# Optimization experiments

Hardware: AMD Instinct MI355X
Metric: run time of the kernel (lower is better)

Reference implementation:

```python
import jax, jax.numpy as jnp
import numpy as np

VOCAB = 32000
D = 256
B, S = 16, 128


def setup_inputs() -> dict:
    key = jax.random.key(0)
    ks = jax.random.split(key, 8)
    s = 1.0 / np.sqrt(D)
    return {
        "X": jax.random.randint(ks[0], (B, S), 0, VOCAB),
        "emb": jax.random.normal(ks[1], (VOCAB, D), dtype=jnp.float32),
        "Wl": jax.random.uniform(ks[2], (D, D), jnp.float32, -s, s),
        "bl": jax.random.uniform(ks[3], (D,), jnp.float32, -s, s),
        "Wr": jax.random.uniform(ks[4], (D, D), jnp.float32, -s, s),
        "br": jax.random.uniform(ks[5], (D,), jnp.float32, -s, s),
        "Wrel": jax.random.uniform(ks[6], (D, D), jnp.float32, -s, s),
        "brel": jax.random.uniform(ks[7], (D,), jnp.float32, -s, s),
    }


def reference(X, emb, Wl, bl, Wr, br, Wrel, brel):
    # X: [B,S] int -> embed [B,S,D]
    e = emb[X]
    L = jnp.einsum("bsd,de->bse", e, Wl.T) + bl  # left projection per token
    R = jnp.einsum("bsd,de->bse", e, Wr.T) + br  # right projection per token
    # all-pairs relu(L_i + R_j): [B,S,S,D]
    pair = jax.nn.relu(L[:, :, None, :] + R[:, None, :, :])
    # relation is affine, so mean over S^2 pairs commutes with it (same math,
    # one [B,D] GEMM instead of B*S^2 tiny ones)
    pooled = pair.mean(axis=(1, 2))  # [B,D]
    return pooled @ Wrel.T + brel
```

## Files before the change

kernel.cpp:

```cpp
#include <hip/hip_runtime.h>
#include <hip/hip_bf16.h>

#define DD 256
#define SS 128
#define BB 16

typedef __attribute__((ext_vector_type(8))) short bf16x8;
typedef __attribute__((ext_vector_type(4))) short bf16x4;
typedef __attribute__((ext_vector_type(4))) float f32x4;

static __device__ __forceinline__ short f2bf(float f) {
    __hip_bfloat16 h = __float2bfloat16(f);
    return *reinterpret_cast<short*>(&h);
}

static __device__ __forceinline__ int swz(int r, int kb) {
    return r * 512 + (kb ^ ((r & 7) << 4));
}


__global__ __launch_bounds__(512, 2) void k_fused(
    const int* __restrict__ X, const float* __restrict__ emb,
    const float* __restrict__ Wl, const float* __restrict__ bl,
    const float* __restrict__ Wr, const float* __restrict__ br,
    float* __restrict__ sumLg, float* __restrict__ sumRg,
    float* __restrict__ absS)
{
    __shared__ __align__(16) short Ebf[128 * 256];
    __shared__ __align__(16) float Lcol[16 * 132];
    __shared__ __align__(16) float Rcol[16 * 132];
    __shared__ float redA[512];
    __shared__ float redwL[8 * 16];
    __shared__ float redwR[8 * 16];

    const int tid  = threadIdx.x;
    const int bx   = (blockIdx.x & 7) * 32 + (blockIdx.x >> 3);
    const int b    = bx >> 4;
    const int dc   = bx & 15;
    const int dr0  = dc * 16;
    const int w    = __builtin_amdgcn_readfirstlane(tid >> 6);
    const int lane = tid & 63;
    const int lr   = lane & 15, lk = lane >> 4;

    int tok[16];
#pragma unroll
    for (int i = 0; i < 8; ++i) tok[i]     = X[b * SS + i * 8 + w];
#pragma unroll
    for (int i = 0; i < 8; ++i) tok[8 + i] = X[b * SS + 64 + i * 8 + w];

    float4 ga[16];
#pragma unroll
    for (int i = 0; i < 16; ++i)
        ga[i] = *(const float4*)&emb[(size_t)tok[i] * DD + lane * 4];

    bf16x8 wlf[8], wrf[8];
    {
        const float* plw = Wl + (size_t)(dr0 + lr) * DD + lk * 8;
        const float* prw = Wr + (size_t)(dr0 + lr) * DD + lk * 8;
#pragma unroll
        for (int ks = 0; ks < 8; ++ks) {
            float4 f0 = *(const float4*)(plw + ks * 32);
            float4 f1 = *(const float4*)(plw + ks * 32 + 4);
            bf16x8 p;
            p[0]=f2bf(f0.x); p[1]=f2bf(f0.y); p[2]=f2bf(f0.z); p[3]=f2bf(f0.w);
            p[4]=f2bf(f1.x); p[5]=f2bf(f1.y); p[6]=f2bf(f1.z); p[7]=f2bf(f1.w);
            wlf[ks] = p;
            f0 = *(const float4*)(prw + ks * 32);
            f1 = *(const float4*)(prw + ks * 32 + 4);
            p[0]=f2bf(f0.x); p[1]=f2bf(f0.y); p[2]=f2bf(f0.z); p[3]=f2bf(f0.w);
            p[4]=f2bf(f1.x); p[5]=f2bf(f1.y); p[6]=f2bf(f1.z); p[7]=f2bf(f1.w);
            wrf[ks] = p;
        }
    }

    char* Eb = (char*)Ebf;
#pragma unroll
    for (int i = 0; i < 8; ++i) {
        bf16x4 p; p[0]=f2bf(ga[i].x); p[1]=f2bf(ga[i].y); p[2]=f2bf(ga[i].z); p[3]=f2bf(ga[i].w);
        *(bf16x4*)(Eb + swz(i * 8 + w, lane * 8)) = p;
    }
#pragma unroll
    for (int i = 0; i < 8; ++i) {
        bf16x4 p; p[0]=f2bf(ga[8+i].x); p[1]=f2bf(ga[8+i].y); p[2]=f2bf(ga[8+i].z); p[3]=f2bf(ga[8+i].w);
        *(bf16x4*)(Eb + swz(64 + i * 8 + w, lane * 8)) = p;
    }
    __syncthreads();

    f32x4 accL = {0.f,0.f,0.f,0.f}, accR = accL;
#pragma unroll
    for (int ks = 0; ks < 8; ++ks) {
        bf16x8 a = *(bf16x8*)(Eb + swz(w * 16 + lr, ks * 64 + lk * 16));
        accL = __builtin_amdgcn_mfma_f32_16x16x32_bf16(a, wlf[ks], accL, 0, 0, 0);
        accR = __builtin_amdgcn_mfma_f32_16x16x32_bf16(a, wrf[ks], accR, 0, 0, 0);
    }
    const float blv = bl[dr0 + lr];
    const float brv = br[dr0 + lr];
#pragma unroll
    for (int reg = 0; reg < 4; ++reg) {
        int s = w * 16 + lk * 4 + reg;
        Lcol[lr * 132 + s] = accL[reg] + blv;
        Rcol[lr * 132 + s] = accR[reg] + brv;
    }
    float tl = (accL[0] + accL[1]) + (accL[2] + accL[3]) + blv * 4.0f;
    float tr = (accR[0] + accR[1]) + (accR[2] + accR[3]) + brv * 4.0f;
    tl += __shfl_xor(tl, 16);  tr += __shfl_xor(tr, 16);
    tl += __shfl_xor(tl, 32);  tr += __shfl_xor(tr, 32);
    if (lane < 16) { redwL[w * 16 + lr] = tl; redwR[w * 16 + lr] = tr; }
    __syncthreads();

    const int d = tid & 15, jg = tid >> 4;
    float rr[4];
    *(float4*)rr = *(float4*)&Rcol[d * 132 + jg * 4];

    float a0 = 0.f, a1 = 0.f, a2 = 0.f, a3 = 0.f;
    for (int i = 0; i < 128; i += 4) {
        float4 l4 = *(float4*)&Lcol[d * 132 + i];
#pragma unroll
        for (int q = 0; q < 4; ++q) {
            a0 += fabsf(l4.x + rr[q]);
            a1 += fabsf(l4.y + rr[q]);
            a2 += fabsf(l4.z + rr[q]);
            a3 += fabsf(l4.w + rr[q]);
        }
    }
    redA[tid] = (a0 + a1) + (a2 + a3);
    __syncthreads();

    if (tid < 16) {
        float sa = 0.f;
#pragma unroll
        for (int g = 0; g < 32; ++g) sa += redA[g * 16 + tid];
        float sl = 0.f, sr = 0.f;
#pragma unroll
        for (int wv = 0; wv < 8; ++wv) {
            sl += redwL[wv * 16 + tid];
            sr += redwR[wv * 16 + tid];
        }
        absS [b * DD + dr0 + tid] = sa;
        sumLg[b * DD + dr0 + tid] = sl;
        sumRg[b * DD + dr0 + tid] = sr;
    }
}

__global__ __launch_bounds__(256) void k_final(
    const float* __restrict__ sumLg, const float* __restrict__ sumRg,
    const float* __restrict__ absS,
    const float* __restrict__ Wrel, const float* __restrict__ brel,
    float* __restrict__ out)
{
    __shared__ float plds[DD];
    const int tid = threadIdx.x;
    const int b   = blockIdx.x;

    float sl = sumLg[b * DD + tid];
    float sr = sumRg[b * DD + tid];
    float sa = absS [b * DD + tid];

    plds[tid] = (128.0f * (sl + sr) + sa) * (1.0f / 32768.0f);
    __syncthreads();

    float acc = brel[tid];
    const float4* w4 = (const float4*)(Wrel + (size_t)tid * DD);
#pragma unroll
    for (int k4 = 0; k4 < DD / 4; ++k4) {
        float4 p = *(float4*)&plds[k4 * 4];
        float4 w = w4[k4];
        acc = fmaf(p.x, w.x, acc);
        acc = fmaf(p.y, w.y, acc);
        acc = fmaf(p.z, w.z, acc);
        acc = fmaf(p.w, w.w, acc);
    }
    out[b * DD + tid] = acc;
}

extern "C" void kernel_launch(void* const* d_in, const int* in_sizes, int n_in,
                              void* d_out, int out_size, void* d_ws, size_t ws_size,
                              hipStream_t stream) {
    const int*   X    = (const int*)d_in[0];
    const float* emb  = (const float*)d_in[1];
    const float* Wl   = (const float*)d_in[2];
    const float* bl   = (const float*)d_in[3];
    const float* Wr   = (const float*)d_in[4];
    const float* br   = (const float*)d_in[5];
    const float* Wrel = (const float*)d_in[6];
    const float* brel = (const float*)d_in[7];
    float* out = (float*)d_out;

    float* ws    = (float*)d_ws;
    float* sumLg = ws;
    float* sumRg = sumLg + BB * DD;
    float* absS  = sumRg + BB * DD;

    k_fused<<<BB * 16, 512, 0, stream>>>(X, emb, Wl, bl, Wr, br,
                                         sumLg, sumRg, absS);
    k_final<<<BB, 256, 0, stream>>>(sumLg, sumRg, absS, Wrel, brel, out);
}
```

Measured before the change: 27.89 us.

## Gather embeddings straight into LDS via global_load_lds; split-K the final GEMV

The embedding gather now uses global_load_lds to copy fp32 rows directly into LDS. The XOR swizzle is applied on the global source address, and each wave waits on vmcnt for only its own rows, replacing the register staging, bf16 conversion and block barrier. The bf16 conversion moves to the MFMA operand load, and LDS storage doubles to fp32, which limits the fused kernel to one block per CU. The final Wrel GEMV uses 1024 threads with a 4-way K split and preloaded weights to shorten the per-thread dependent FMA chain.

Result: slower. 28.46 us (+2.1%).

```diff
diff --git a/kernel.cpp b/kernel.cpp
--- a/kernel.cpp
+++ b/kernel.cpp
@@ -6,7 +6,6 @@
 #define BB 16
 
 typedef __attribute__((ext_vector_type(8))) short bf16x8;
-typedef __attribute__((ext_vector_type(4))) short bf16x4;
 typedef __attribute__((ext_vector_type(4))) float f32x4;
 
 static __device__ __forceinline__ short f2bf(float f) {
@@ -14,19 +13,22 @@
     return *reinterpret_cast<short*>(&h);
 }
 
-static __device__ __forceinline__ int swz(int r, int kb) {
-    return r * 512 + (kb ^ ((r & 7) << 4));
-}
-
-
-__global__ __launch_bounds__(512, 2) void k_fused(
+static __device__ __forceinline__ void gl_lds16(const float* g, float* l) {
+    __builtin_amdgcn_global_load_lds(
+        (const __attribute__((address_space(1))) void*)g,
+        (__attribute__((address_space(3))) void*)l,
+        16, 0, 0);
+}
+
+
+__global__ __launch_bounds__(512) void k_fused(
     const int* __restrict__ X, const float* __restrict__ emb,
     const float* __restrict__ Wl, const float* __restrict__ bl,
     const float* __restrict__ Wr, const float* __restrict__ br,
     float* __restrict__ sumLg, float* __restrict__ sumRg,
     float* __restrict__ absS)
 {
-    __shared__ __align__(16) short Ebf[128 * 256];
+    __shared__ __align__(16) float Ef[128 * 256];
     __shared__ __align__(16) float Lcol[16 * 132];
     __shared__ __align__(16) float Rcol[16 * 132];
     __shared__ float redA[512];
@@ -38,20 +40,17 @@
     const int b    = bx >> 4;
     const int dc   = bx & 15;
     const int dr0  = dc * 16;
-    const int w    = __builtin_amdgcn_readfirstlane(tid >> 6);
+    const int w    = tid >> 6;
     const int lane = tid & 63;
     const int lr   = lane & 15, lk = lane >> 4;
 
-    int tok[16];
-#pragma unroll
-    for (int i = 0; i < 8; ++i) tok[i]     = X[b * SS + i * 8 + w];
-#pragma unroll
-    for (int i = 0; i < 8; ++i) tok[8 + i] = X[b * SS + 64 + i * 8 + w];
-
-    float4 ga[16];
-#pragma unroll
-    for (int i = 0; i < 16; ++i)
-        ga[i] = *(const float4*)&emb[(size_t)tok[i] * DD + lane * 4];
+#pragma unroll
+    for (int i = 0; i < 16; ++i) {
+        const int r   = w * 16 + i;
+        const int tok = X[b * SS + r];
+        const float* g = emb + (size_t)tok * DD + ((lane ^ (r & 7)) << 2);
+        gl_lds16(g, &Ef[r * 256]);
+    }
 
     bf16x8 wlf[8], wrf[8];
     {
@@ -73,23 +72,19 @@
         }
     }
 
-    char* Eb = (char*)Ebf;
-#pragma unroll
-    for (int i = 0; i < 8; ++i) {
-        bf16x4 p; p[0]=f2bf(ga[i].x); p[1]=f2bf(ga[i].y); p[2]=f2bf(ga[i].z); p[3]=f2bf(ga[i].w);
-        *(bf16x4*)(Eb + swz(i * 8 + w, lane * 8)) = p;
-    }
-#pragma unroll
-    for (int i = 0; i < 8; ++i) {
-        bf16x4 p; p[0]=f2bf(ga[8+i].x); p[1]=f2bf(ga[8+i].y); p[2]=f2bf(ga[8+i].z); p[3]=f2bf(ga[8+i].w);
-        *(bf16x4*)(Eb + swz(64 + i * 8 + w, lane * 8)) = p;
-    }
-    __syncthreads();
+    asm volatile("s_waitcnt vmcnt(0)" ::: "memory");
 
     f32x4 accL = {0.f,0.f,0.f,0.f}, accR = accL;
+    const float* Erow = &Ef[(size_t)(w * 16 + lr) * 256];
+    const int xw = lr & 7;
 #pragma unroll
     for (int ks = 0; ks < 8; ++ks) {
-        bf16x8 a = *(bf16x8*)(Eb + swz(w * 16 + lr, ks * 64 + lk * 16));
+        const int c0 = ks * 8 + lk * 2;
+        float4 fa = *(const float4*)&Erow[(c0 ^ xw) << 2];
+        float4 fb = *(const float4*)&Erow[((c0 + 1) ^ xw) << 2];
+        bf16x8 a;
+        a[0]=f2bf(fa.x); a[1]=f2bf(fa.y); a[2]=f2bf(fa.z); a[3]=f2bf(fa.w);
+        a[4]=f2bf(fb.x); a[5]=f2bf(fb.y); a[6]=f2bf(fb.z); a[7]=f2bf(fb.w);
         accL = __builtin_amdgcn_mfma_f32_16x16x32_bf16(a, wlf[ks], accL, 0, 0, 0);
         accR = __builtin_amdgcn_mfma_f32_16x16x32_bf16(a, wrf[ks], accR, 0, 0, 0);
     }
@@ -142,35 +137,47 @@
     }
 }
 
-__global__ __launch_bounds__(256) void k_final(
+__global__ __launch_bounds__(1024) void k_final(
     const float* __restrict__ sumLg, const float* __restrict__ sumRg,
     const float* __restrict__ absS,
     const float* __restrict__ Wrel, const float* __restrict__ brel,
     float* __restrict__ out)
 {
     __shared__ float plds[DD];
+    __shared__ float part[4][256];
     const int tid = threadIdx.x;
     const int b   = blockIdx.x;
-
-    float sl = sumLg[b * DD + tid];
-    float sr = sumRg[b * DD + tid];
-    float sa = absS [b * DD + tid];
-
-    plds[tid] = (128.0f * (sl + sr) + sa) * (1.0f / 32768.0f);
-    __syncthreads();
-
-    float acc = brel[tid];
-    const float4* w4 = (const float4*)(Wrel + (size_t)tid * DD);
-#pragma unroll
-    for (int k4 = 0; k4 < DD / 4; ++k4) {
-        float4 p = *(float4*)&plds[k4 * 4];
-        float4 w = w4[k4];
-        acc = fmaf(p.x, w.x, acc);
-        acc = fmaf(p.y, w.y, acc);
-        acc = fmaf(p.z, w.z, acc);
-        acc = fmaf(p.w, w.w, acc);
-    }
-    out[b * DD + tid] = acc;
+    const int row = tid & 255, q = tid >> 8;
+
+    if (tid < DD) {
+        float sl = sumLg[b * DD + tid];
+        float sr = sumRg[b * DD + tid];
+        float sa = absS [b * DD + tid];
+        plds[tid] = (128.0f * (sl + sr) + sa) * (1.0f / 32768.0f);
+    }
+
+    const float4* w4 = (const float4*)(Wrel + (size_t)row * DD + q * 64);
+    float4 wr[16];
+#pragma unroll
+    for (int i = 0; i < 16; ++i) wr[i] = w4[i];
+
+    __syncthreads();
+
+    float acc = 0.f;
+#pragma unroll
+    for (int i = 0; i < 16; ++i) {
+        float4 p = *(float4*)&plds[q * 64 + i * 4];
+        acc = fmaf(wr[i].x, p.x, acc);
+        acc = fmaf(wr[i].y, p.y, acc);
+        acc = fmaf(wr[i].z, p.z, acc);
+        acc = fmaf(wr[i].w, p.w, acc);
+    }
+    part[q][row] = acc;
+    __syncthreads();
+
+    if (tid < 256)
+        out[b * DD + tid] = brel[tid] +
+            ((part[0][tid] + part[1][tid]) + (part[2][tid] + part[3][tid]));
 }
 
 extern "C" void kernel_launch(void* const* d_in, const int* in_sizes, int n_in,
@@ -193,5 +200,5 @@
 
     k_fused<<<BB * 16, 512, 0, stream>>>(X, emb, Wl, bl, Wr, br,
                                          sumLg, sumRg, absS);
-    k_final<<<BB, 256, 0, stream>>>(sumLg, sumRg, absS, Wrel, brel, out);
-}
+    k_final<<<BB, 1024, 0, stream>>>(sumLg, sumRg, absS, Wrel, brel, out);
+}
```
